# Performance work log

Hardware: AMD Instinct MI355X
Metric: run time of the kernel (lower is better)

The kernel has to match this reference:

```python
import jax, jax.numpy as jnp
import numpy as np

MAXDISP = 48
GROUP = 8
EPS = 1e-5


def setup_inputs() -> dict:
    key = jax.random.key(0)
    k1, k2 = jax.random.split(key)
    x = jax.random.normal(k1, (2, 64, 96, 320), dtype=jnp.float32)
    y = jax.random.normal(k2, (2, 64, 96, 320), dtype=jnp.float32)
    return {"x": x, "y": y}


def reference(x, y):
    # Faithful translation of CostVolume.forward.
    # torch's unfold over left-zero-padded y at kernel position d picks
    # y_pad[..., j + d]; per-window L2 norm over channels reduces to a
    # per-pixel channel norm (padded zeros normalize to zero), so we
    # normalize once and gather shifted columns.
    D = MAXDISP + 1
    b, c, h, w = x.shape
    cpg = c // GROUP
    xg = x.reshape(b, GROUP, cpg, h, w)
    yg = y.reshape(b, GROUP, cpg, h, w)
    xn = xg / (jnp.linalg.norm(xg, axis=2, keepdims=True) + EPS)
    yn = yg / (jnp.linalg.norm(yg, axis=2, keepdims=True) + EPS)
    # left zero-pad width dim by MAXDISP (padded zeros stay zero after norm)
    y_pad = jnp.pad(yn, ((0, 0), (0, 0), (0, 0), (0, 0), (MAXDISP, 0)))
    # after torch.flip on the disparity axis, disparity k compares x[:, j]
    # with y[:, j - k]  ->  padded index j + MAXDISP - k
    idx = jnp.arange(w)[None, :] + MAXDISP - jnp.arange(D)[:, None]  # [D, w]
    y_shift = y_pad[..., idx]  # [b, g, cpg, h, D, w]
    cost = jnp.sum(jnp.abs(xn[:, :, :, :, None, :] - y_shift), axis=2)  # [b,g,h,D,w]
    return jnp.transpose(cost, (0, 1, 3, 2, 4))  # [b, group, D, h, w]
```

## Files before the change

### kernel.cpp

```cpp
#include <hip/hip_runtime.h>


#define MAXDISP 48
#define NDISP   49
#define HH      96
#define WW      320
#define EPSN    1e-5f

__global__ __launch_bounds__(WW) void cost_volume_kernel(
    const float* __restrict__ x, const float* __restrict__ y,
    float* __restrict__ out)
{
    __shared__ float4 ylds[2 * WW];

    const int j   = threadIdx.x;
    const int blk = blockIdx.x;
    const int h   = blk % HH;
    const int bg  = blk / HH;

    const int inBase = bg * 8 * (HH * WW) + h * WW + j;

    float xv[8], yv[8];
    float xs = 0.f, ys = 0.f;
#pragma unroll
    for (int cc = 0; cc < 8; ++cc) {
        float xi = x[inBase + cc * (HH * WW)];
        float yi = y[inBase + cc * (HH * WW)];
        xv[cc] = xi; yv[cc] = yi;
        xs += xi * xi;
        ys += yi * yi;
    }
    const float xinv = 1.f / (sqrtf(xs) + EPSN);
    const float yinv = 1.f / (sqrtf(ys) + EPSN);

    float sAbs = 0.f;
#pragma unroll
    for (int cc = 0; cc < 8; ++cc) {
        xv[cc] *= xinv;
        yv[cc] *= yinv;
        sAbs += fabsf(xv[cc]);
    }

    ylds[j]      = make_float4(yv[0], yv[1], yv[2], yv[3]);
    ylds[WW + j] = make_float4(yv[4], yv[5], yv[6], yv[7]);
    __syncthreads();

    float* outp = out + bg * (NDISP * HH * WW) + h * WW + j;

#pragma unroll 7
    for (int d = 0; d < NDISP; ++d) {
        float cost;
        const int jj = j - d;
        if (jj >= 0) {
            const float4 a = ylds[jj];
            const float4 b = ylds[WW + jj];
            cost = fabsf(xv[0] - a.x) + fabsf(xv[1] - a.y)
                 + fabsf(xv[2] - a.z) + fabsf(xv[3] - a.w)
                 + fabsf(xv[4] - b.x) + fabsf(xv[5] - b.y)
                 + fabsf(xv[6] - b.z) + fabsf(xv[7] - b.w);
        } else {
            cost = sAbs;
        }
        outp[d * (HH * WW)] = cost;
    }
}

extern "C" void kernel_launch(void* const* d_in, const int* in_sizes, int n_in,
                              void* d_out, int out_size, void* d_ws, size_t ws_size,
                              hipStream_t stream) {
    const float* x = (const float*)d_in[0];
    const float* y = (const float*)d_in[1];
    float* out = (float*)d_out;
    dim3 grid(2 * 8 * HH);
    dim3 block(WW);
    cost_volume_kernel<<<grid, block, 0, stream>>>(x, y, out);
}
```

Before: 127.6 us.

## Compute two adjacent pixels per thread with register-reused shifted y values

```diff
diff --git a/kernel.cpp b/kernel.cpp
--- a/kernel.cpp
+++ b/kernel.cpp
@@ -5,63 +5,90 @@
 #define NDISP   49
 #define HH      96
 #define WW      320
+#define HW      (HH * WW)
 #define EPSN    1e-5f
 
-__global__ __launch_bounds__(WW) void cost_volume_kernel(
+__global__ __launch_bounds__(320) void cost_volume_kernel(
     const float* __restrict__ x, const float* __restrict__ y,
     float* __restrict__ out)
 {
-    __shared__ float4 ylds[2 * WW];
+    __shared__ float4 ylds[2][2][2][WW / 2];
 
-    const int j   = threadIdx.x;
+    const int tid = threadIdx.x;
+    const int q   = tid % 160;
+    const int r   = tid / 160;
+    const int j   = 2 * q;
+
     const int blk = blockIdx.x;
-    const int h   = blk % HH;
-    const int bg  = blk / HH;
+    const int hp  = blk % (HH / 2);
+    const int bg  = blk / (HH / 2);
+    const int h   = hp * 2 + r;
 
-    const int inBase = bg * 8 * (HH * WW) + h * WW + j;
+    const int inBase = bg * 8 * HW + h * WW + j;
 
-    float xv[8], yv[8];
-    float xs = 0.f, ys = 0.f;
+    float xa[8], xb[8], ya[8], yb[8];
+    float xsa = 0.f, xsb = 0.f, ysa = 0.f, ysb = 0.f;
 #pragma unroll
     for (int cc = 0; cc < 8; ++cc) {
-        float xi = x[inBase + cc * (HH * WW)];
-        float yi = y[inBase + cc * (HH * WW)];
-        xv[cc] = xi; yv[cc] = yi;
-        xs += xi * xi;
-        ys += yi * yi;
+        const float2 xi = *reinterpret_cast<const float2*>(x + inBase + cc * HW);
+        const float2 yi = *reinterpret_cast<const float2*>(y + inBase + cc * HW);
+        xa[cc] = xi.x; xb[cc] = xi.y;
+        ya[cc] = yi.x; yb[cc] = yi.y;
+        xsa += xi.x * xi.x; xsb += xi.y * xi.y;
+        ysa += yi.x * yi.x; ysb += yi.y * yi.y;
     }
-    const float xinv = 1.f / (sqrtf(xs) + EPSN);
-    const float yinv = 1.f / (sqrtf(ys) + EPSN);
+    const float xia = 1.f / (sqrtf(xsa) + EPSN);
+    const float xib = 1.f / (sqrtf(xsb) + EPSN);
+    const float yia = 1.f / (sqrtf(ysa) + EPSN);
+    const float yib = 1.f / (sqrtf(ysb) + EPSN);
 
-    float sAbs = 0.f;
+    float sAbsA = 0.f, sAbsB = 0.f;
 #pragma unroll
     for (int cc = 0; cc < 8; ++cc) {
-        xv[cc] *= xinv;
-        yv[cc] *= yinv;
-        sAbs += fabsf(xv[cc]);
+        xa[cc] *= xia; xb[cc] *= xib;
+        ya[cc] *= yia; yb[cc] *= yib;
+        sAbsA += fabsf(xa[cc]);
+        sAbsB += fabsf(xb[cc]);
     }
 
-    ylds[j]      = make_float4(yv[0], yv[1], yv[2], yv[3]);
-    ylds[WW + j] = make_float4(yv[4], yv[5], yv[6], yv[7]);
+    ylds[r][0][0][q] = make_float4(ya[0], ya[1], ya[2], ya[3]);
+    ylds[r][0][1][q] = make_float4(ya[4], ya[5], ya[6], ya[7]);
+    ylds[r][1][0][q] = make_float4(yb[0], yb[1], yb[2], yb[3]);
+    ylds[r][1][1][q] = make_float4(yb[4], yb[5], yb[6], yb[7]);
     __syncthreads();
 
-    float* outp = out + bg * (NDISP * HH * WW) + h * WW + j;
+    const float4* ldsE = &ylds[r][0][0][0];
+    const float4* ldsO = &ylds[r][1][0][0];
+
+    float4 yp0 = ldsE[q],       yp1 = ldsE[160 + q];
+    float4 yc0 = ldsO[q],       yc1 = ldsO[160 + q];
+
+    const float4* bcur = ldsO;
+    const float4* bnxt = ldsE;
+
+    float* outp = out + bg * (NDISP * HW) + h * WW + j;
 
 #pragma unroll 7
     for (int d = 0; d < NDISP; ++d) {
-        float cost;
-        const int jj = j - d;
-        if (jj >= 0) {
-            const float4 a = ylds[jj];
-            const float4 b = ylds[WW + jj];
-            cost = fabsf(xv[0] - a.x) + fabsf(xv[1] - a.y)
-                 + fabsf(xv[2] - a.z) + fabsf(xv[3] - a.w)
-                 + fabsf(xv[4] - b.x) + fabsf(xv[5] - b.y)
-                 + fabsf(xv[6] - b.z) + fabsf(xv[7] - b.w);
-        } else {
-            cost = sAbs;
-        }
-        outp[d * (HH * WW)] = cost;
+        float c0 = fabsf(xa[0] - yp0.x) + fabsf(xa[1] - yp0.y)
+                 + fabsf(xa[2] - yp0.z) + fabsf(xa[3] - yp0.w)
+                 + fabsf(xa[4] - yp1.x) + fabsf(xa[5] - yp1.y)
+                 + fabsf(xa[6] - yp1.z) + fabsf(xa[7] - yp1.w);
+        float c1 = fabsf(xb[0] - yc0.x) + fabsf(xb[1] - yc0.y)
+                 + fabsf(xb[2] - yc0.z) + fabsf(xb[3] - yc0.w)
+                 + fabsf(xb[4] - yc1.x) + fabsf(xb[5] - yc1.y)
+                 + fabsf(xb[6] - yc1.z) + fabsf(xb[7] - yc1.w);
+        c0 = (d <= j)     ? c0 : sAbsA;
+        c1 = (d <= j + 1) ? c1 : sAbsB;
+        *reinterpret_cast<float2*>(outp) = make_float2(c0, c1);
+        outp += HW;
+
+        yc0 = yp0; yc1 = yp1;
+        const int pn  = j - d - 1;
+        const int idx = (pn > 0 ? pn : 0) >> 1;
+        yp0 = bcur[idx];
+        yp1 = bcur[160 + idx];
+        const float4* t = bcur; bcur = bnxt; bnxt = t;
     }
 }
 
@@ -71,7 +98,7 @@
     const float* x = (const float*)d_in[0];
     const float* y = (const float*)d_in[1];
     float* out = (float*)d_out;
-    dim3 grid(2 * 8 * HH);
-    dim3 block(WW);
+    dim3 grid(2 * 8 * (HH / 2));
+    dim3 block(320);
     cost_volume_kernel<<<grid, block, 0, stream>>>(x, y, out);
 }
```

Measured after the change: 132.9 us. 1.04x slower.
